# Performance work log

Measured on AMD Instinct MI355X. Metric: run time of the kernel, lower is better.

## Reference

```python
import jax, jax.numpy as jnp
import numpy as np

B, S, D = 2, 2048, 2048
H, KV, HD = 16, 4, 128  # n_heads, n_kv_heads, head_dim
N_REP = H // KV
ROPE_THETA = 10000.0


def setup_inputs() -> dict:
    key = jax.random.key(0)
    ks = jax.random.split(key, 5)
    sc = 1.0 / np.sqrt(D).astype(np.float32)
    x = jax.random.normal(ks[0], (B, S, D), jnp.float32)
    wq = jax.random.normal(ks[1], (D, H * HD), jnp.float32) * sc
    wk = jax.random.normal(ks[2], (D, KV * HD), jnp.float32) * sc
    wv = jax.random.normal(ks[3], (D, KV * HD), jnp.float32) * sc
    wo = jax.random.normal(ks[4], (H * HD, D), jnp.float32) * sc
    # freqs_cis = exp(i * t * theta^(-2j/d)) represented as cos/sin, shape (S, HD//2)
    inv_freq = 1.0 / (ROPE_THETA ** (np.arange(0, HD, 2, dtype=np.float32) / HD))
    ang = np.outer(np.arange(S, dtype=np.float32), inv_freq)
    return {
        "x": x, "wq": wq, "wk": wk, "wv": wv, "wo": wo,
        "freqs_cos": jnp.asarray(np.cos(ang), jnp.float32),
        "freqs_sin": jnp.asarray(np.sin(ang), jnp.float32),
    }


def _rope(t, cos, sin):
    # t: [B, S, h, HD]; pairs (t[...,2i], t[...,2i+1]) form complex numbers
    tr = t.reshape(t.shape[:-1] + (HD // 2, 2))
    re, im = tr[..., 0], tr[..., 1]
    c = cos[None, :, None, :]
    s = sin[None, :, None, :]
    out = jnp.stack([re * c - im * s, re * s + im * c], axis=-1)
    return out.reshape(t.shape)


def reference(x, wq, wk, wv, wo, freqs_cos, freqs_sin):
    b, s, _ = x.shape
    xq = (x @ wq).reshape(b, s, H, HD)
    xk = (x @ wk).reshape(b, s, KV, HD)
    xv = (x @ wv).reshape(b, s, KV, HD)
    xq = _rope(xq, freqs_cos, freqs_sin)
    xk = _rope(xk, freqs_cos, freqs_sin)
    # repeat_kv: each kv head repeated N_REP times consecutively
    keys = jnp.repeat(xk, N_REP, axis=2)    # [b, s, H, HD]
    vals = jnp.repeat(xv, N_REP, axis=2)
    q = xq.transpose(0, 2, 1, 3)            # [b, H, s, HD]
    k = keys.transpose(0, 2, 1, 3)
    v = vals.transpose(0, 2, 1, 3)
    scores = jnp.einsum('bhqd,bhkd->bhqk', q, k) / np.sqrt(HD).astype(np.float32)
    mask = jnp.triu(jnp.full((s, s), -jnp.inf, dtype=jnp.float32), k=1)
    probs = jax.nn.softmax(scores + mask, axis=-1)
    out = jnp.einsum('bhqk,bhkd->bhqd', probs, v)
    out = out.transpose(0, 2, 1, 3).reshape(b, s, H * HD)
    return out @ wo
```

## Files before the change

### kernel.cpp

```cpp
#include <hip/hip_runtime.h>

typedef __attribute__((ext_vector_type(8))) short bf16x8;
typedef __attribute__((ext_vector_type(4))) float f32x4;
typedef __attribute__((ext_vector_type(4))) unsigned short u16x4;

#define DI __device__ __forceinline__

constexpr int CB = 2, CS = 2048, CD = 2048, CH = 16, CKV = 4, CHD = 128;

DI unsigned short f2bf(float f) {
  unsigned u = __builtin_bit_cast(unsigned, f);
  u += 0x7fffu + ((u >> 16) & 1u);
  return (unsigned short)(u >> 16);
}
DI float bf2f(unsigned short h) {
  return __builtin_bit_cast(float, (unsigned)h << 16);
}

#define GLOAD16(g, l) __builtin_amdgcn_global_load_lds(                      \
    (const __attribute__((address_space(1))) unsigned*)(g),                  \
    (__attribute__((address_space(3))) unsigned*)(l), 16, 0, 0)

__global__ __launch_bounds__(256) void cvt_bf16(const float* __restrict__ in,
                                                unsigned short* __restrict__ out)
{
  const size_t i = ((size_t)blockIdx.x * 256 + threadIdx.x) * 8;
  const float4 a = *(const float4*)&in[i];
  const float4 b = *(const float4*)&in[i + 4];
  bf16x8 v;
  v[0] = f2bf(a.x); v[1] = f2bf(a.y); v[2] = f2bf(a.z); v[3] = f2bf(a.w);
  v[4] = f2bf(b.x); v[5] = f2bf(b.y); v[6] = f2bf(b.z); v[7] = f2bf(b.w);
  *(bf16x8*)&out[i] = v;
}

__global__ __launch_bounds__(256) void cvtT_bf16(const float* __restrict__ W,
                                                 unsigned short* __restrict__ Wt,
                                                 int K, int N)
{
  __shared__ __align__(16) unsigned short Ls[64][72];
  const int n0 = blockIdx.x * 64, k0 = blockIdx.y * 64;
  const int t = threadIdx.x;
  const int r = t >> 4, c = (t & 15) << 2;
#pragma unroll
  for (int ph = 0; ph < 4; ++ph) {
    const int row = ph * 16 + r;
    const float4 f = *(const float4*)&W[(size_t)(k0 + row) * N + n0 + c];
    Ls[c + 0][row] = f2bf(f.x);
    Ls[c + 1][row] = f2bf(f.y);
    Ls[c + 2][row] = f2bf(f.z);
    Ls[c + 3][row] = f2bf(f.w);
  }
  __syncthreads();
  const int wr = t >> 2, wc = (t & 3) << 4;
  const bf16x8 v0 = *(const bf16x8*)&Ls[wr][wc];
  const bf16x8 v1 = *(const bf16x8*)&Ls[wr][wc + 8];
  *(bf16x8*)&Wt[(size_t)(n0 + wr) * K + k0 + wc]     = v0;
  *(bf16x8*)&Wt[(size_t)(n0 + wr) * K + k0 + wc + 8] = v1;
}

template <int MODE>
__global__ __launch_bounds__(256) void gemm_bt(
    const unsigned short* __restrict__ A, const unsigned short* __restrict__ Bt,
    void* __restrict__ Cptr, unsigned short* __restrict__ K2,
    unsigned short* __restrict__ V2, int M, int N, int K)
{
  __shared__ __align__(16) unsigned short As[128 * 32];
  __shared__ __align__(16) unsigned short Bs[128 * 32];

  const int t = threadIdx.x;
  const int w = t >> 6, l = t & 63;
  const int l15 = l & 15, lg = l >> 4;
  const int wr = w >> 1, wc = w & 1;
  const int m0 = blockIdx.y * 128;
  const int n0 = blockIdx.x * 128;

  const int sr = l >> 2, sc = (l & 3) << 3;
  const unsigned short* aSrc0 = A  + (size_t)(m0 + w * 16 + sr) * K + sc;
  const unsigned short* aSrc1 = A  + (size_t)(m0 + 64 + w * 16 + sr) * K + sc;
  const unsigned short* bSrc0 = Bt + (size_t)(n0 + w * 16 + sr) * K + sc;
  const unsigned short* bSrc1 = Bt + (size_t)(n0 + 64 + w * 16 + sr) * K + sc;
  unsigned short* aDst0 = As + (w * 16) * 32;
  unsigned short* aDst1 = As + (64 + w * 16) * 32;
  unsigned short* bDst0 = Bs + (w * 16) * 32;
  unsigned short* bDst1 = Bs + (64 + w * 16) * 32;

  f32x4 acc[4][4];
#pragma unroll
  for (int i = 0; i < 4; ++i)
#pragma unroll
    for (int j = 0; j < 4; ++j) acc[i][j] = (f32x4){0.f, 0.f, 0.f, 0.f};

  for (int kt = 0; kt < K; kt += 32) {
    GLOAD16(aSrc0 + kt, aDst0);
    GLOAD16(aSrc1 + kt, aDst1);
    GLOAD16(bSrc0 + kt, bDst0);
    GLOAD16(bSrc1 + kt, bDst1);
    __syncthreads();

    bf16x8 aF[4], bF[4];
#pragma unroll
    for (int i = 0; i < 4; ++i) {
      aF[i] = *(const bf16x8*)&As[(wr * 64 + i * 16 + l15) * 32 + lg * 8];
      bF[i] = *(const bf16x8*)&Bs[(wc * 64 + i * 16 + l15) * 32 + lg * 8];
    }
#pragma unroll
    for (int mi = 0; mi < 4; ++mi)
#pragma unroll
      for (int ni = 0; ni < 4; ++ni)
        acc[mi][ni] = __builtin_amdgcn_mfma_f32_16x16x32_bf16(aF[mi], bF[ni], acc[mi][ni], 0, 0, 0);

    __syncthreads();
  }

  unsigned short* dst16 = nullptr;
  int cstr = N, coff = n0;
  if (MODE == 2) {
    if (n0 < 2048)      { dst16 = (unsigned short*)Cptr; cstr = 2048; coff = n0; }
    else if (n0 < 2560) { dst16 = K2; cstr = 512; coff = n0 - 2048; }
    else                { dst16 = V2; cstr = 512; coff = n0 - 2560; }
  }
#pragma unroll
  for (int mi = 0; mi < 4; ++mi) {
    const int row0 = m0 + wr * 64 + mi * 16 + lg * 4;
#pragma unroll
    for (int j = 0; j < 4; ++j) {
#pragma unroll
      for (int ni = 0; ni < 4; ++ni) {
        const int cl = wc * 64 + ni * 16 + l15;
        const float v = acc[mi][ni][j];
        if (MODE == 0)
          ((float*)Cptr)[(size_t)(row0 + j) * N + n0 + cl] = v;
        else if (MODE == 1)
          ((unsigned short*)Cptr)[(size_t)(row0 + j) * N + n0 + cl] = f2bf(v);
        else
          dst16[(size_t)(row0 + j) * cstr + coff + cl] = f2bf(v);
      }
    }
  }
}

__global__ void rope_bf16(unsigned short* __restrict__ tq,
                          const float* __restrict__ cosT,
                          const float* __restrict__ sinT,
                          int nH, float scale, int total)
{
  int idx = blockIdx.x * blockDim.x + threadIdx.x;
  if (idx >= total) return;
  const int p    = idx & 63;
  const int rest = idx >> 6;
  const int s    = (rest / nH) & (CS - 1);
  const float c  = cosT[s * 64 + p];
  const float sn = sinT[s * 64 + p];
  unsigned short* ptr = tq + (size_t)rest * CHD;
  const unsigned pair = *(const unsigned*)&ptr[2 * p];
  const float re = bf2f((unsigned short)pair);
  const float im = bf2f((unsigned short)(pair >> 16));
  const unsigned short lo = f2bf((re * c - im * sn) * scale);
  const unsigned short hi = f2bf((re * sn + im * c) * scale);
  *(unsigned*)&ptr[2 * p] = (unsigned)lo | ((unsigned)hi << 16);
}

__global__ __launch_bounds__(256) void attn_mfma(
    const unsigned short* __restrict__ Qb, const unsigned short* __restrict__ Kb,
    const unsigned short* __restrict__ Vb, unsigned short* __restrict__ Ob)
{
  constexpr int KSTR = 136, VSTR = 72, PSTR = 72, NT = CS / 64;
  __shared__ __align__(16) unsigned short KsB[64 * KSTR];
  __shared__ __align__(16) unsigned short VtB[128 * VSTR];
  __shared__ __align__(16) unsigned short PsB[4 * 16 * PSTR];

  const int t   = threadIdx.x;
  const int w   = t >> 6, l = t & 63;
  const int l15 = l & 15, lg = l >> 4;
  const int g = blockIdx.x, h = blockIdx.y, b = blockIdx.z;
  const int kvh = h >> 2;

  const int skr = t >> 2, skc = (t & 3) << 5;

  bf16x8 kpre[4];
  u16x4  vpre0[4], vpre1[4];

#define ATTN_PREFETCH(KT)                                                          \
  {                                                                                \
    const unsigned short* ksrc =                                                   \
        Kb + ((size_t)(b * CS + (KT) + skr) * CKV + kvh) * CHD + skc;              \
    _Pragma("unroll") for (int i = 0; i < 4; ++i)                                  \
        kpre[i] = *(const bf16x8*)&ksrc[i * 8];                                    \
    _Pragma("unroll") for (int ii = 0; ii < 4; ++ii) {                             \
      const int idx = t + 256 * ii;                                                \
      const int kp = idx & 31, dg = idx >> 5;                                      \
      const unsigned short* vsrc =                                                 \
          Vb + ((size_t)(b * CS + (KT) + kp * 2) * CKV + kvh) * CHD + dg * 4;      \
      vpre0[ii] = *(const u16x4*)vsrc;                                             \
      vpre1[ii] = *(const u16x4*)(vsrc + (size_t)CKV * CHD);                       \
    }                                                                              \
  }

#define ATTN_WRITE_LDS                                                             \
  {                                                                                \
    _Pragma("unroll") for (int i = 0; i < 4; ++i)                                  \
        *(bf16x8*)&KsB[skr * KSTR + skc + i * 8] = kpre[i];                        \
    _Pragma("unroll") for (int ii = 0; ii < 4; ++ii) {                             \
      const int idx = t + 256 * ii;                                                \
      const int kp = idx & 31, dg = idx >> 5;                                      \
      const int r = kp * 2;                                                        \
      _Pragma("unroll") for (int c2 = 0; c2 < 4; ++c2)                             \
        *(unsigned*)&VtB[(dg * 4 + c2) * VSTR + r] =                               \
            (unsigned)(unsigned short)vpre0[ii][c2] |                              \
            ((unsigned)(unsigned short)vpre1[ii][c2] << 16);                       \
    }                                                                              \
  }

#pragma unroll 1
  for (int qi = 0; qi < 2; ++qi) {
    const int qt = qi ? (NT - 1 - g) : g;
    const int q0 = qt * 64;

    bf16x8 qf[4];
    {
      const size_t qrow = ((size_t)(b * CS + q0 + w * 16 + l15) * CH + h) * CHD;
#pragma unroll
      for (int kk = 0; kk < 4; ++kk)
        qf[kk] = *(const bf16x8*)&Qb[qrow + kk * 32 + lg * 8];
    }

    f32x4 accO[8];
#pragma unroll
    for (int i = 0; i < 8; ++i) accO[i] = (f32x4){0.f, 0.f, 0.f, 0.f};
    float m_j[4] = {-1e30f, -1e30f, -1e30f, -1e30f};
    float l_j[4] = {0.f, 0.f, 0.f, 0.f};

    ATTN_PREFETCH(0);

    for (int kt = 0; kt <= q0; kt += 64) {
      __syncthreads();
      ATTN_WRITE_LDS;
      if (kt + 64 <= q0) ATTN_PREFETCH(kt + 64);
      __syncthreads();

      f32x4 s[4];
#pragma unroll
      for (int ks = 0; ks < 4; ++ks) s[ks] = (f32x4){0.f, 0.f, 0.f, 0.f};
#pragma unroll
      for (int kk = 0; kk < 4; ++kk)
#pragma unroll
        for (int ks = 0; ks < 4; ++ks) {
          const bf16x8 bf = *(const bf16x8*)&KsB[(ks * 16 + l15) * KSTR + kk * 32 + lg * 8];
          s[ks] = __builtin_amdgcn_mfma_f32_16x16x32_bf16(qf[kk], bf, s[ks], 0, 0, 0);
        }

      if (kt == q0) {
        const int qr = q0 + w * 16 + lg * 4;
#pragma unroll
        for (int ks = 0; ks < 4; ++ks) {
          const int kg = kt + ks * 16 + l15;
#pragma unroll
          for (int j = 0; j < 4; ++j)
            if (kg > qr + j) s[ks][j] = -1e30f;
        }
      }

      float rs[4];
#pragma unroll
      for (int j = 0; j < 4; ++j) {
        float mx = fmaxf(fmaxf(s[0][j], s[1][j]), fmaxf(s[2][j], s[3][j]));
        mx = fmaxf(mx, __shfl_xor(mx, 1));
        mx = fmaxf(mx, __shfl_xor(mx, 2));
        mx = fmaxf(mx, __shfl_xor(mx, 4));
        mx = fmaxf(mx, __shfl_xor(mx, 8));
        const float mnew = fmaxf(m_j[j], mx);
        float sum = 0.f;
#pragma unroll
        for (int ks = 0; ks < 4; ++ks) {
          const float p = __expf(s[ks][j] - mnew);
          s[ks][j] = p;
          sum += p;
        }
        sum += __shfl_xor(sum, 1);
        sum += __shfl_xor(sum, 2);
        sum += __shfl_xor(sum, 4);
        sum += __shfl_xor(sum, 8);
        rs[j]  = __expf(m_j[j] - mnew);
        l_j[j] = l_j[j] * rs[j] + sum;
        m_j[j] = mnew;
      }
#pragma unroll
      for (int d8 = 0; d8 < 8; ++d8)
#pragma unroll
        for (int j = 0; j < 4; ++j) accO[d8][j] *= rs[j];

      unsigned short* Pw = PsB + w * 16 * PSTR;
#pragma unroll
      for (int ks = 0; ks < 4; ++ks)
#pragma unroll
        for (int j = 0; j < 4; ++j)
          Pw[(lg * 4 + j) * PSTR + ks * 16 + l15] = f2bf(s[ks][j]);

#pragma unroll
      for (int k2 = 0; k2 < 2; ++k2) {
        const bf16x8 pa = *(const bf16x8*)&Pw[l15 * PSTR + k2 * 32 + lg * 8];
#pragma unroll
        for (int d8 = 0; d8 < 8; ++d8) {
          const bf16x8 bv = *(const bf16x8*)&VtB[(d8 * 16 + l15) * VSTR + k2 * 32 + lg * 8];
          accO[d8] = __builtin_amdgcn_mfma_f32_16x16x32_bf16(pa, bv, accO[d8], 0, 0, 0);
        }
      }
    }

#pragma unroll
    for (int j = 0; j < 4; ++j) {
      const float inv = 1.f / l_j[j];
      const size_t base = ((size_t)(b * CS + q0 + w * 16 + lg * 4 + j) * CH + h) * CHD;
#pragma unroll
      for (int d8 = 0; d8 < 8; ++d8)
        Ob[base + d8 * 16 + l15] = f2bf(accO[d8][j] * inv);
    }
  }
#undef ATTN_PREFETCH
#undef ATTN_WRITE_LDS
}

extern "C" void kernel_launch(void* const* d_in, const int* in_sizes, int n_in,
                              void* d_out, int out_size, void* d_ws, size_t ws_size,
                              hipStream_t stream)
{
  const float* x  = (const float*)d_in[0];
  const float* wq = (const float*)d_in[1];
  const float* wk = (const float*)d_in[2];
  const float* wv = (const float*)d_in[3];
  const float* wo = (const float*)d_in[4];
  const float* fc = (const float*)d_in[5];
  const float* fs = (const float*)d_in[6];
  float* out = (float*)d_out;

  unsigned short* qb = (unsigned short*)d_ws;
  unsigned short* kb = qb + (size_t)CB * CS * CH * CHD;
  unsigned short* vb = kb + (size_t)CB * CS * CKV * CHD;
  unsigned short* wt = vb + (size_t)CB * CS * CKV * CHD;
  unsigned short* xb = (unsigned short*)d_out;

  const int M = CB * CS;
  dim3 blk(256);

  cvt_bf16<<<dim3((CB * CS * CD) / (256 * 8)), blk, 0, stream>>>(x, xb);

  cvtT_bf16<<<dim3(CD / 64, CD / 64), blk, 0, stream>>>(wq, wt, CD, CD);
  cvtT_bf16<<<dim3((CKV * CHD) / 64, CD / 64), blk, 0, stream>>>(wk, wt + (size_t)2048 * CD, CD, CKV * CHD);
  cvtT_bf16<<<dim3((CKV * CHD) / 64, CD / 64), blk, 0, stream>>>(wv, wt + (size_t)2560 * CD, CD, CKV * CHD);

  gemm_bt<2><<<dim3(3072 / 128, M / 128), blk, 0, stream>>>(xb, wt, qb, kb, vb, M, 3072, CD);

  const int qpairs = CB * CS * CH * (CHD / 2);
  const int kpairs = CB * CS * CKV * (CHD / 2);
  rope_bf16<<<(qpairs + 255) / 256, 256, 0, stream>>>(qb, fc, fs, CH, 0.08838834764831845f, qpairs);
  rope_bf16<<<(kpairs + 255) / 256, 256, 0, stream>>>(kb, fc, fs, CKV, 1.0f, kpairs);

  attn_mfma<<<dim3(CS / 128, CH, CB), blk, 0, stream>>>(qb, kb, vb, qb);

  cvtT_bf16<<<dim3(CD / 64, CD / 64), blk, 0, stream>>>(wo, wt, CD, CD);
  gemm_bt<0><<<dim3(CD / 128, M / 128), blk, 0, stream>>>(qb, wt, out, nullptr, nullptr, M, CD, CD);
}
```

Baseline: 368.6 us.

## Double attention query tile per block, remap GEMM blocks for L2 locality

The attention kernel now processes 128 query rows per block, 32 per wave as two 16-row subtiles. Each K/V tile loaded into LDS is reused by twice as many MFMAs, and the grid is halved to 8x16x2 blocks. Wave priority hints are placed around the MFMA sections. The GEMM block index is remapped in an 8-way interleave that changes which output tiles run together, aiming for better cache locality. The trade-off is higher register pressure, possible lower occupancy, and fewer blocks for the causal load balancing.

```diff
diff --git a/kernel.cpp b/kernel.cpp
--- a/kernel.cpp
+++ b/kernel.cpp
@@ -71,8 +71,13 @@
   const int w = t >> 6, l = t & 63;
   const int l15 = l & 15, lg = l >> 4;
   const int wr = w >> 1, wc = w & 1;
-  const int m0 = blockIdx.y * 128;
-  const int n0 = blockIdx.x * 128;
+
+  const int gx = gridDim.x;
+  int lid = blockIdx.x + gx * blockIdx.y;
+  const int cpx = (gx * gridDim.y) >> 3;
+  lid = (lid & 7) * cpx + (lid >> 3);
+  const int m0 = (lid / gx) * 128;
+  const int n0 = (lid % gx) * 128;
 
   const int sr = l >> 2, sc = (l & 3) << 3;
   const unsigned short* aSrc0 = A  + (size_t)(m0 + w * 16 + sr) * K + sc;
@@ -130,8 +135,6 @@
         const float v = acc[mi][ni][j];
         if (MODE == 0)
           ((float*)Cptr)[(size_t)(row0 + j) * N + n0 + cl] = v;
-        else if (MODE == 1)
-          ((unsigned short*)Cptr)[(size_t)(row0 + j) * N + n0 + cl] = f2bf(v);
         else
           dst16[(size_t)(row0 + j) * cstr + coff + cl] = f2bf(v);
       }
@@ -164,10 +167,10 @@
     const unsigned short* __restrict__ Qb, const unsigned short* __restrict__ Kb,
     const unsigned short* __restrict__ Vb, unsigned short* __restrict__ Ob)
 {
-  constexpr int KSTR = 136, VSTR = 72, PSTR = 72, NT = CS / 64;
+  constexpr int KSTR = 136, VSTR = 72, PSTR = 72, NT = CS / 128;
   __shared__ __align__(16) unsigned short KsB[64 * KSTR];
   __shared__ __align__(16) unsigned short VtB[128 * VSTR];
-  __shared__ __align__(16) unsigned short PsB[4 * 16 * PSTR];
+  __shared__ __align__(16) unsigned short PsB[4 * 32 * PSTR];
 
   const int t   = threadIdx.x;
   const int w   = t >> 6, l = t & 63;
@@ -214,107 +217,127 @@
 #pragma unroll 1
   for (int qi = 0; qi < 2; ++qi) {
     const int qt = qi ? (NT - 1 - g) : g;
-    const int q0 = qt * 64;
-
-    bf16x8 qf[4];
-    {
-      const size_t qrow = ((size_t)(b * CS + q0 + w * 16 + l15) * CH + h) * CHD;
+    const int q0 = qt * 128;
+    const int last = q0 + 64;
+
+    bf16x8 qf[2][4];
+#pragma unroll
+    for (int rt = 0; rt < 2; ++rt) {
+      const size_t qrow = ((size_t)(b * CS + q0 + w * 32 + rt * 16 + l15) * CH + h) * CHD;
 #pragma unroll
       for (int kk = 0; kk < 4; ++kk)
-        qf[kk] = *(const bf16x8*)&Qb[qrow + kk * 32 + lg * 8];
+        qf[rt][kk] = *(const bf16x8*)&Qb[qrow + kk * 32 + lg * 8];
     }
 
-    f32x4 accO[8];
-#pragma unroll
-    for (int i = 0; i < 8; ++i) accO[i] = (f32x4){0.f, 0.f, 0.f, 0.f};
-    float m_j[4] = {-1e30f, -1e30f, -1e30f, -1e30f};
-    float l_j[4] = {0.f, 0.f, 0.f, 0.f};
+    f32x4 accO[2][8];
+#pragma unroll
+    for (int rt = 0; rt < 2; ++rt)
+#pragma unroll
+      for (int i = 0; i < 8; ++i) accO[rt][i] = (f32x4){0.f, 0.f, 0.f, 0.f};
+    float m_j[2][4], l_j[2][4];
+#pragma unroll
+    for (int rt = 0; rt < 2; ++rt)
+#pragma unroll
+      for (int j = 0; j < 4; ++j) { m_j[rt][j] = -1e30f; l_j[rt][j] = 0.f; }
 
     ATTN_PREFETCH(0);
 
-    for (int kt = 0; kt <= q0; kt += 64) {
+    for (int kt = 0; kt <= last; kt += 64) {
       __syncthreads();
       ATTN_WRITE_LDS;
-      if (kt + 64 <= q0) ATTN_PREFETCH(kt + 64);
+      if (kt + 64 <= last) ATTN_PREFETCH(kt + 64);
       __syncthreads();
 
-      f32x4 s[4];
-#pragma unroll
-      for (int ks = 0; ks < 4; ++ks) s[ks] = (f32x4){0.f, 0.f, 0.f, 0.f};
-#pragma unroll
-      for (int kk = 0; kk < 4; ++kk)
-#pragma unroll
-        for (int ks = 0; ks < 4; ++ks) {
-          const bf16x8 bf = *(const bf16x8*)&KsB[(ks * 16 + l15) * KSTR + kk * 32 + lg * 8];
-          s[ks] = __builtin_amdgcn_mfma_f32_16x16x32_bf16(qf[kk], bf, s[ks], 0, 0, 0);
+      unsigned short* Pw = PsB + w * 32 * PSTR;
+
+#pragma unroll
+      for (int rt = 0; rt < 2; ++rt) {
+        f32x4 s[4];
+#pragma unroll
+        for (int ks = 0; ks < 4; ++ks) s[ks] = (f32x4){0.f, 0.f, 0.f, 0.f};
+        __builtin_amdgcn_s_setprio(1);
+#pragma unroll
+        for (int kk = 0; kk < 4; ++kk)
+#pragma unroll
+          for (int ks = 0; ks < 4; ++ks) {
+            const bf16x8 bf = *(const bf16x8*)&KsB[(ks * 16 + l15) * KSTR + kk * 32 + lg * 8];
+            s[ks] = __builtin_amdgcn_mfma_f32_16x16x32_bf16(qf[rt][kk], bf, s[ks], 0, 0, 0);
+          }
+        __builtin_amdgcn_s_setprio(0);
+
+        if (kt + 64 > q0) {
+          const int qr = q0 + w * 32 + rt * 16 + lg * 4;
+#pragma unroll
+          for (int ks = 0; ks < 4; ++ks) {
+            const int kg = kt + ks * 16 + l15;
+#pragma unroll
+            for (int j = 0; j < 4; ++j)
+              if (kg > qr + j) s[ks][j] = -1e30f;
+          }
         }
 
-      if (kt == q0) {
-        const int qr = q0 + w * 16 + lg * 4;
-#pragma unroll
-        for (int ks = 0; ks < 4; ++ks) {
-          const int kg = kt + ks * 16 + l15;
+        float rs[4];
+#pragma unroll
+        for (int j = 0; j < 4; ++j) {
+          float mx = fmaxf(fmaxf(s[0][j], s[1][j]), fmaxf(s[2][j], s[3][j]));
+          mx = fmaxf(mx, __shfl_xor(mx, 1));
+          mx = fmaxf(mx, __shfl_xor(mx, 2));
+          mx = fmaxf(mx, __shfl_xor(mx, 4));
+          mx = fmaxf(mx, __shfl_xor(mx, 8));
+          const float mnew = fmaxf(m_j[rt][j], mx);
+          float sum = 0.f;
+#pragma unroll
+          for (int ks = 0; ks < 4; ++ks) {
+            const float p = __expf(s[ks][j] - mnew);
+            s[ks][j] = p;
+            sum += p;
+          }
+          sum += __shfl_xor(sum, 1);
+          sum += __shfl_xor(sum, 2);
+          sum += __shfl_xor(sum, 4);
+          sum += __shfl_xor(sum, 8);
+          rs[j]      = __expf(m_j[rt][j] - mnew);
+          l_j[rt][j] = l_j[rt][j] * rs[j] + sum;
+          m_j[rt][j] = mnew;
+        }
+#pragma unroll
+        for (int d8 = 0; d8 < 8; ++d8)
+#pragma unroll
+          for (int j = 0; j < 4; ++j) accO[rt][d8][j] *= rs[j];
+
+#pragma unroll
+        for (int ks = 0; ks < 4; ++ks)
 #pragma unroll
           for (int j = 0; j < 4; ++j)
-            if (kg > qr + j) s[ks][j] = -1e30f;
+            Pw[(rt * 16 + lg * 4 + j) * PSTR + ks * 16 + l15] = f2bf(s[ks][j]);
+      }
+
+      __builtin_amdgcn_s_setprio(1);
+#pragma unroll
+      for (int k2 = 0; k2 < 2; ++k2) {
+        const bf16x8 pa0 = *(const bf16x8*)&Pw[(l15) * PSTR + k2 * 32 + lg * 8];
+        const bf16x8 pa1 = *(const bf16x8*)&Pw[(16 + l15) * PSTR + k2 * 32 + lg * 8];
+#pragma unroll
+        for (int d8 = 0; d8 < 8; ++d8) {
+          const bf16x8 bv = *(const bf16x8*)&VtB[(d8 * 16 + l15) * VSTR + k2 * 32 + lg * 8];
+          accO[0][d8] = __builtin_amdgcn_mfma_f32_16x16x32_bf16(pa0, bv, accO[0][d8], 0, 0, 0);
+          accO[1][d8] = __builtin_amdgcn_mfma_f32_16x16x32_bf16(pa1, bv, accO[1][d8], 0, 0, 0);
         }
       }
-
-      float rs[4];
+      __builtin_amdgcn_s_setprio(0);
+    }
+
+#pragma unroll
+    for (int rt = 0; rt < 2; ++rt)
 #pragma unroll
       for (int j = 0; j < 4; ++j) {
-        float mx = fmaxf(fmaxf(s[0][j], s[1][j]), fmaxf(s[2][j], s[3][j]));
-        mx = fmaxf(mx, __shfl_xor(mx, 1));
-        mx = fmaxf(mx, __shfl_xor(mx, 2));
-        mx = fmaxf(mx, __shfl_xor(mx, 4));
-        mx = fmaxf(mx, __shfl_xor(mx, 8));
-        const float mnew = fmaxf(m_j[j], mx);
-        float sum = 0.f;
-#pragma unroll
-        for (int ks = 0; ks < 4; ++ks) {
-          const float p = __expf(s[ks][j] - mnew);
-          s[ks][j] = p;
-          sum += p;
-        }
-        sum += __shfl_xor(sum, 1);
-        sum += __shfl_xor(sum, 2);
-        sum += __shfl_xor(sum, 4);
-        sum += __shfl_xor(sum, 8);
-        rs[j]  = __expf(m_j[j] - mnew);
-        l_j[j] = l_j[j] * rs[j] + sum;
-        m_j[j] = mnew;
+        const float inv = 1.f / l_j[rt][j];
+        const size_t base =
+            ((size_t)(b * CS + q0 + w * 32 + rt * 16 + lg * 4 + j) * CH + h) * CHD;
+#pragma unroll
+        for (int d8 = 0; d8 < 8; ++d8)
+          Ob[base + d8 * 16 + l15] = f2bf(accO[rt][d8][j] * inv);
       }
-#pragma unroll
-      for (int d8 = 0; d8 < 8; ++d8)
-#pragma unroll
-        for (int j = 0; j < 4; ++j) accO[d8][j] *= rs[j];
-
-      unsigned short* Pw = PsB + w * 16 * PSTR;
-#pragma unroll
-      for (int ks = 0; ks < 4; ++ks)
-#pragma unroll
-        for (int j = 0; j < 4; ++j)
-          Pw[(lg * 4 + j) * PSTR + ks * 16 + l15] = f2bf(s[ks][j]);
-
-#pragma unroll
-      for (int k2 = 0; k2 < 2; ++k2) {
-        const bf16x8 pa = *(const bf16x8*)&Pw[l15 * PSTR + k2 * 32 + lg * 8];
-#pragma unroll
-        for (int d8 = 0; d8 < 8; ++d8) {
-          const bf16x8 bv = *(const bf16x8*)&VtB[(d8 * 16 + l15) * VSTR + k2 * 32 + lg * 8];
-          accO[d8] = __builtin_amdgcn_mfma_f32_16x16x32_bf16(pa, bv, accO[d8], 0, 0, 0);
-        }
-      }
-    }
-
-#pragma unroll
-    for (int j = 0; j < 4; ++j) {
-      const float inv = 1.f / l_j[j];
-      const size_t base = ((size_t)(b * CS + q0 + w * 16 + lg * 4 + j) * CH + h) * CHD;
-#pragma unroll
-      for (int d8 = 0; d8 < 8; ++d8)
-        Ob[base + d8 * 16 + l15] = f2bf(accO[d8][j] * inv);
-    }
   }
 #undef ATTN_PREFETCH
 #undef ATTN_WRITE_LDS
@@ -355,7 +378,7 @@
   rope_bf16<<<(qpairs + 255) / 256, 256, 0, stream>>>(qb, fc, fs, CH, 0.08838834764831845f, qpairs);
   rope_bf16<<<(kpairs + 255) / 256, 256, 0, stream>>>(kb, fc, fs, CKV, 1.0f, kpairs);
 
-  attn_mfma<<<dim3(CS / 128, CH, CB), blk, 0, stream>>>(qb, kb, vb, qb);
+  attn_mfma<<<dim3(CS / 256, CH, CB), blk, 0, stream>>>(qb, kb, vb, qb);
 
   cvtT_bf16<<<dim3(CD / 64, CD / 64), blk, 0, stream>>>(wo, wt, CD, CD);
   gemm_bt<0><<<dim3(CD / 128, M / 128), blk, 0, stream>>>(qb, wt, out, nullptr, nullptr, M, CD, CD);
```

Result: slower. 392.6 us (+6.5%).

## Double-buffer attention K/V tiles with one barrier per step; swizzle GEMM blocks

Applied to the files above, without the earlier changes.

The attention loop now keeps K and V tiles in two LDS buffers. The next tile is written after the PV MFMAs, so each iteration needs one barrier (an LDS-count wait plus s_barrier) instead of two __syncthreads. The P staging area reuses the idle half of the K buffer, and s_setprio is raised around the MFMA sections to favour matrix issue. The GEMM also remaps block IDs in chunks of 8, presumably to group neighbouring tiles per XCD for better L2 reuse. The MODE 1 store path is removed, and the remap assumes the grid size is divisible by 8.

```diff
diff --git a/kernel.cpp b/kernel.cpp
--- a/kernel.cpp
+++ b/kernel.cpp
@@ -71,8 +71,13 @@
   const int w = t >> 6, l = t & 63;
   const int l15 = l & 15, lg = l >> 4;
   const int wr = w >> 1, wc = w & 1;
-  const int m0 = blockIdx.y * 128;
-  const int n0 = blockIdx.x * 128;
+
+  const int gx = gridDim.x;
+  int lid = blockIdx.x + gx * blockIdx.y;
+  const int cpx = (gx * gridDim.y) >> 3;
+  lid = (lid & 7) * cpx + (lid >> 3);
+  const int m0 = (lid / gx) * 128;
+  const int n0 = (lid % gx) * 128;
 
   const int sr = l >> 2, sc = (l & 3) << 3;
   const unsigned short* aSrc0 = A  + (size_t)(m0 + w * 16 + sr) * K + sc;
@@ -130,8 +135,6 @@
         const float v = acc[mi][ni][j];
         if (MODE == 0)
           ((float*)Cptr)[(size_t)(row0 + j) * N + n0 + cl] = v;
-        else if (MODE == 1)
-          ((unsigned short*)Cptr)[(size_t)(row0 + j) * N + n0 + cl] = f2bf(v);
         else
           dst16[(size_t)(row0 + j) * cstr + coff + cl] = f2bf(v);
       }
@@ -164,10 +167,10 @@
     const unsigned short* __restrict__ Qb, const unsigned short* __restrict__ Kb,
     const unsigned short* __restrict__ Vb, unsigned short* __restrict__ Ob)
 {
-  constexpr int KSTR = 136, VSTR = 72, PSTR = 72, NT = CS / 64;
-  __shared__ __align__(16) unsigned short KsB[64 * KSTR];
-  __shared__ __align__(16) unsigned short VtB[128 * VSTR];
-  __shared__ __align__(16) unsigned short PsB[4 * 16 * PSTR];
+  constexpr int KSTR = 136, VSTR = 72, NT = CS / 64;
+  constexpr int KOFF = 64 * KSTR, VOFF = 128 * VSTR;
+  __shared__ __align__(16) unsigned short KbB[2 * KOFF];
+  __shared__ __align__(16) unsigned short VtL[2 * VOFF];
 
   const int t   = threadIdx.x;
   const int w   = t >> 6, l = t & 63;
@@ -196,25 +199,32 @@
     }                                                                              \
   }
 
-#define ATTN_WRITE_LDS                                                             \
+#define ATTN_WRITE_LDS(BUF)                                                        \
   {                                                                                \
+    unsigned short* kdst = KbB + (BUF) * KOFF;                                     \
+    unsigned short* vdst = VtL + (BUF) * VOFF;                                     \
     _Pragma("unroll") for (int i = 0; i < 4; ++i)                                  \
-        *(bf16x8*)&KsB[skr * KSTR + skc + i * 8] = kpre[i];                        \
+        *(bf16x8*)&kdst[skr * KSTR + skc + i * 8] = kpre[i];                       \
     _Pragma("unroll") for (int ii = 0; ii < 4; ++ii) {                             \
       const int idx = t + 256 * ii;                                                \
       const int kp = idx & 31, dg = idx >> 5;                                      \
       const int r = kp * 2;                                                        \
       _Pragma("unroll") for (int c2 = 0; c2 < 4; ++c2)                             \
-        *(unsigned*)&VtB[(dg * 4 + c2) * VSTR + r] =                               \
+        *(unsigned*)&vdst[(dg * 4 + c2) * VSTR + r] =                              \
             (unsigned)(unsigned short)vpre0[ii][c2] |                              \
             ((unsigned)(unsigned short)vpre1[ii][c2] << 16);                       \
     }                                                                              \
   }
+
+#define ATTN_BAR                                                                   \
+  asm volatile("s_waitcnt lgkmcnt(0)" ::: "memory");                               \
+  __builtin_amdgcn_s_barrier();
 
 #pragma unroll 1
   for (int qi = 0; qi < 2; ++qi) {
     const int qt = qi ? (NT - 1 - g) : g;
     const int q0 = qt * 64;
+    const int nt = q0 / 64 + 1;
 
     bf16x8 qf[4];
     {
@@ -231,23 +241,29 @@
     float l_j[4] = {0.f, 0.f, 0.f, 0.f};
 
     ATTN_PREFETCH(0);
-
-    for (int kt = 0; kt <= q0; kt += 64) {
-      __syncthreads();
-      ATTN_WRITE_LDS;
-      if (kt + 64 <= q0) ATTN_PREFETCH(kt + 64);
-      __syncthreads();
+    ATTN_WRITE_LDS(0);
+    if (nt > 1) ATTN_PREFETCH(64);
+    ATTN_BAR;
+
+    int cur = 0;
+    for (int ti = 0; ti < nt; ++ti) {
+      const int kt = ti * 64;
+      const unsigned short* Ks = KbB + cur * KOFF;
+      const unsigned short* Vt = VtL + cur * VOFF;
+      unsigned short* Pw = KbB + (cur ^ 1) * KOFF + (w * 16) * KSTR;
 
       f32x4 s[4];
 #pragma unroll
       for (int ks = 0; ks < 4; ++ks) s[ks] = (f32x4){0.f, 0.f, 0.f, 0.f};
+      __builtin_amdgcn_s_setprio(1);
 #pragma unroll
       for (int kk = 0; kk < 4; ++kk)
 #pragma unroll
         for (int ks = 0; ks < 4; ++ks) {
-          const bf16x8 bf = *(const bf16x8*)&KsB[(ks * 16 + l15) * KSTR + kk * 32 + lg * 8];
+          const bf16x8 bf = *(const bf16x8*)&Ks[(ks * 16 + l15) * KSTR + kk * 32 + lg * 8];
           s[ks] = __builtin_amdgcn_mfma_f32_16x16x32_bf16(qf[kk], bf, s[ks], 0, 0, 0);
         }
+      __builtin_amdgcn_s_setprio(0);
 
       if (kt == q0) {
         const int qr = q0 + w * 16 + lg * 4;
@@ -289,22 +305,30 @@
 #pragma unroll
         for (int j = 0; j < 4; ++j) accO[d8][j] *= rs[j];
 
-      unsigned short* Pw = PsB + w * 16 * PSTR;
 #pragma unroll
       for (int ks = 0; ks < 4; ++ks)
 #pragma unroll
         for (int j = 0; j < 4; ++j)
-          Pw[(lg * 4 + j) * PSTR + ks * 16 + l15] = f2bf(s[ks][j]);
-
+          Pw[(lg * 4 + j) * KSTR + ks * 16 + l15] = f2bf(s[ks][j]);
+
+      __builtin_amdgcn_s_setprio(1);
 #pragma unroll
       for (int k2 = 0; k2 < 2; ++k2) {
-        const bf16x8 pa = *(const bf16x8*)&Pw[l15 * PSTR + k2 * 32 + lg * 8];
+        const bf16x8 pa = *(const bf16x8*)&Pw[l15 * KSTR + k2 * 32 + lg * 8];
 #pragma unroll
         for (int d8 = 0; d8 < 8; ++d8) {
-          const bf16x8 bv = *(const bf16x8*)&VtB[(d8 * 16 + l15) * VSTR + k2 * 32 + lg * 8];
+          const bf16x8 bv = *(const bf16x8*)&Vt[(d8 * 16 + l15) * VSTR + k2 * 32 + lg * 8];
           accO[d8] = __builtin_amdgcn_mfma_f32_16x16x32_bf16(pa, bv, accO[d8], 0, 0, 0);
         }
       }
+      __builtin_amdgcn_s_setprio(0);
+
+      if (ti + 1 < nt) {
+        ATTN_WRITE_LDS(cur ^ 1);
+        if (ti + 2 < nt) ATTN_PREFETCH((ti + 2) * 64);
+      }
+      ATTN_BAR;
+      cur ^= 1;
     }
 
 #pragma unroll
@@ -318,6 +342,7 @@
   }
 #undef ATTN_PREFETCH
 #undef ATTN_WRITE_LDS
+#undef ATTN_BAR
 }
 
 extern "C" void kernel_launch(void* const* d_in, const int* in_sizes, int n_in,
```

Measured after the change: 427.2 us. 15.9% more time.
